# Kernel tuning notes

Measured on AMD Instinct MI355X. Metric: run time of the kernel, lower is better.

## Reference

```python
import jax, jax.numpy as jnp
import numpy as np

K = 3            # pairwise_size
DIL = 2          # pairwise_dilation
COLOR_THR = 0.3  # pairwise_color_thresh
WARMUP = 1.0     # warmup factor (iter >= pairwise_warmup_iters)
COST_CLASS = 1.0
COST_PROJ = 1.0
COST_PAIR = 1.0


def unfold_wo_center(x, k, d):
    # x: (N, T, H, W) -> (N, T, k*k-1, H, W); neighbor at offset (i,j) with dilation d,
    # zero padding, center (i=j=k//2) removed, row-major order (matches F.unfold).
    pad = d * (k - 1) // 2
    H, W = x.shape[-2:]
    xp = jnp.pad(x, ((0, 0), (0, 0), (pad, pad), (pad, pad)))
    outs = []
    for i in range(k):
        for j in range(k):
            if i == k // 2 and j == k // 2:
                continue
            outs.append(xp[..., i * d:i * d + H, j * d:j * d + W])
    return jnp.stack(outs, axis=2)


def batch_dice_loss(inputs, targets):
    # inputs: (N, C), targets: (M, C)
    numerator = 2.0 * jnp.einsum('nc,mc->nm', inputs, targets)
    denominator = inputs.sum(-1)[:, None] + targets.sum(-1)[None, :]
    return 1.0 - (numerator + 1.0) / (denominator + 1.0)


def batch_axis_projection(out_mask, tgt_box_mask, axis):
    # max-project predicted (sigmoid) and box masks along `axis`, dice between projections
    src = jax.nn.sigmoid(out_mask).max(axis=axis).reshape(out_mask.shape[0], -1)
    tgt = tgt_box_mask.max(axis=axis).reshape(tgt_box_mask.shape[0], -1)
    return batch_dice_loss(src, tgt)


def calculate_similarity_cost_video(out_mask, tgt_box_mask, tgt_similarities):
    # out_mask: (Q,T,H,W); tgt_box_mask: (G,T,H,W); tgt_similarities: (G,T,8,H,W)
    Q, T = out_mask.shape[:2]
    G = tgt_box_mask.shape[0]
    tgt_sim = (tgt_similarities >= COLOR_THR).astype(jnp.float32) * tgt_box_mask[:, :, None]
    log_fg = jax.nn.log_sigmoid(out_mask)
    log_bg = jax.nn.log_sigmoid(-out_mask)
    log_fg_u = unfold_wo_center(log_fg, K, DIL)   # (Q,T,8,H,W)
    log_bg_u = unfold_wo_center(log_bg, K, DIL)
    # -log(exp(fg+fg_u) + exp(bg+bg_u)) computed stably
    src_sim = -jnp.logaddexp(log_fg[:, :, None] + log_fg_u,
                             log_bg[:, :, None] + log_bg_u)  # (Q,T,8,H,W)
    src_flat = src_sim.reshape(Q, T, -1)
    tgt_flat = tgt_sim.reshape(G, T, -1)
    numerator = jnp.einsum('qtc,gtc->tqg', src_flat, tgt_flat)      # (T,Q,G)
    denominator = jnp.clip(tgt_flat.sum(-1), 1.0, None)             # (G,T)
    cost = numerator / denominator.T[:, None, :]                    # (T,Q,G)
    return cost.mean(axis=0)                                        # (Q,G)


def setup_inputs() -> dict:
    key = jax.random.key(0)
    k1, k2, k3, k4, k5 = jax.random.split(key, 5)
    Q, G, T, H, W, C = 100, 16, 2, 128, 128, 81
    return {
        'pred_logits': jax.random.normal(k1, (Q, C), dtype=jnp.float32),
        'out_mask': jax.random.normal(k2, (Q, T, H, W), dtype=jnp.float32),
        'tgt_similarities': jax.random.uniform(k3, (G, T, K * K - 1, H, W), dtype=jnp.float32),
        'tgt_ids': jax.random.randint(k4, (G,), 0, C, dtype=jnp.int32),
        'tgt_box_mask': jax.random.randint(k5, (G, T, H, W), 0, 2, dtype=jnp.int32),
    }


def reference(pred_logits, out_mask, tgt_similarities, tgt_ids, tgt_box_mask):
    tgt_box_f = tgt_box_mask.astype(jnp.float32)
    out_prob = jax.nn.softmax(pred_logits, axis=-1)
    cost_class = -out_prob[:, tgt_ids]                                  # (Q,G)
    cost_projection = (batch_axis_projection(out_mask, tgt_box_f, 3)
                       + batch_axis_projection(out_mask, tgt_box_f, 2))  # (Q,G)
    cost_pairwise = calculate_similarity_cost_video(out_mask, tgt_box_f, tgt_similarities) * WARMUP
    C = COST_CLASS * cost_class + COST_PROJ * cost_projection + COST_PAIR * cost_pairwise
    return C
```

## Files before the change

kernel.cpp:

```cpp
#include <hip/hip_runtime.h>
#include <hip/hip_fp16.h>
#include <cstdint>

#define Q_ 100
#define G_ 16
#define T_ 2
#define H_ 128
#define W_ 128
#define HW_ (H_*W_)
#define C_ 81
#define RS_ 69
#define QS_ 553

typedef _Float16 half8 __attribute__((ext_vector_type(8)));
typedef float floatx4 __attribute__((ext_vector_type(4)));

__device__ __forceinline__ float sig_(float x) { return 1.0f / (1.0f + __expf(-x)); }

__launch_bounds__(256)
__global__ void k_prep(const float* __restrict__ om,
                       const int* __restrict__ box,
                       const float* __restrict__ sims,
                       float* __restrict__ srcMW,
                       float* __restrict__ srcMHp,
                       int* __restrict__ tgtMWi,
                       int* __restrict__ tgtMHp,
                       uint32_t* __restrict__ packed,
                       int* __restrict__ cnt_part) {
    __shared__ float credF[128];
    __shared__ int redI[4][4];
    int bid = blockIdx.x;
    int tid = threadIdx.x;

    if (bid < 800) {
        int qt = bid >> 2;
        int rg = bid & 3;
        const float* base = om + (size_t)qt * HW_ + rg * 32 * W_;
        {
            int r = tid >> 3, seg = tid & 7;
            const float4* rp = (const float4*)(base + r * W_ + seg * 16);
            float m = -1e30f;
            #pragma unroll
            for (int i = 0; i < 4; ++i) {
                float4 v = rp[i];
                m = fmaxf(m, fmaxf(fmaxf(v.x, v.y), fmaxf(v.z, v.w)));
            }
            m = fmaxf(m, __shfl_xor(m, 1, 64));
            m = fmaxf(m, __shfl_xor(m, 2, 64));
            m = fmaxf(m, __shfl_xor(m, 4, 64));
            if (seg == 0) srcMW[qt * 128 + rg * 32 + r] = m;
        }
        {
            int c = tid & 127, rh = tid >> 7;
            const float* cp = base + rh * 16 * W_ + c;
            float m = -1e30f;
            #pragma unroll
            for (int i = 0; i < 16; ++i) m = fmaxf(m, cp[i * W_]);
            if (rh == 1) credF[c] = m;
            __syncthreads();
            if (rh == 0) srcMHp[(qt * 4 + rg) * 128 + c] = fmaxf(m, credF[c]);
        }
    } else if (bid < 1056) {
        int b2 = bid - 800;
        int gt = b2 >> 3;
        int rg = b2 & 7;
        const int* base = box + (size_t)gt * HW_ + rg * 16 * W_;
        {
            int r = tid >> 4, seg = tid & 15;
            const int4* rp = (const int4*)(base + r * W_ + seg * 8);
            int4 a = rp[0], b = rp[1];
            int m = max(max(max(a.x, a.y), max(a.z, a.w)),
                        max(max(b.x, b.y), max(b.z, b.w)));
            m = max(m, __shfl_xor(m, 1, 64));
            m = max(m, __shfl_xor(m, 2, 64));
            m = max(m, __shfl_xor(m, 4, 64));
            m = max(m, __shfl_xor(m, 8, 64));
            if (seg == 0) tgtMWi[gt * 128 + rg * 16 + r] = m;
        }
        {
            int* credi = (int*)credF;
            int c = tid & 127, rh = tid >> 7;
            const int* cp = base + rh * 8 * W_ + c;
            int m = 0;
            #pragma unroll
            for (int i = 0; i < 8; ++i) m = max(m, cp[i * W_]);
            if (rh == 1) credi[c] = m;
            __syncthreads();
            if (rh == 0) tgtMHp[(gt * 8 + rg) * 128 + c] = max(m, credi[c]);
        }
    } else {
        int b3 = bid - 1056;
        int gg = b3 & 3;
        int pxblk = b3 >> 2;
        int p0 = pxblk * 512 + tid * 2;
        int t = p0 >> 14;
        int pp = p0 & (HW_ - 1);

        uint32_t w0 = 0, w1 = 0;
        int pc[4];
        #pragma unroll
        for (int b = 0; b < 4; ++b) {
            int g = gg * 4 + b;
            const float* sbase = sims + ((size_t)(g * T_ + t) * 8) * HW_ + pp;
            int2 bx = *(const int2*)(box + (size_t)(g * T_ + t) * HW_ + pp);
            uint32_t by0 = 0, by1 = 0;
            #pragma unroll
            for (int e = 0; e < 8; ++e) {
                float2 sv = *(const float2*)(sbase + (size_t)e * HW_);
                by0 |= (sv.x >= 0.3f ? 1u : 0u) << e;
                by1 |= (sv.y >= 0.3f ? 1u : 0u) << e;
            }
            by0 = bx.x ? by0 : 0u;
            by1 = bx.y ? by1 : 0u;
            w0 |= by0 << (b * 8);
            w1 |= by1 << (b * 8);
            pc[b] = __popc(by0) + __popc(by1);
        }
        *(uint2*)&packed[(size_t)gg * (T_ * HW_) + p0] = make_uint2(w0, w1);

        int wid = tid >> 6, lane = tid & 63;
        #pragma unroll
        for (int b = 0; b < 4; ++b) {
            int s = pc[b];
            #pragma unroll
            for (int o = 32; o > 0; o >>= 1) s += __shfl_down(s, o, 64);
            if (lane == 0) redI[wid][b] = s;
        }
        __syncthreads();
        if (tid < 4)
            cnt_part[pxblk * 16 + gg * 4 + tid] =
                redI[0][tid] + redI[1][tid] + redI[2][tid] + redI[3][tid];
    }
}

__global__ void k_dice(const float* __restrict__ logits, const int* __restrict__ ids,
                       const float* __restrict__ srcMW, const float* __restrict__ srcMHp,
                       const int* __restrict__ tgtMWi, const int* __restrict__ tgtMHp,
                       const int* __restrict__ cnt_part,
                       int* __restrict__ cntF,
                       float* __restrict__ out) {
    int q = blockIdx.x >> 4;
    int g = blockIdx.x & 15;
    int l = threadIdx.x;

    if (q == 0) {
        int tt = l >> 5, pb = l & 31;
        int v = cnt_part[(tt * 32 + pb) * 16 + g];
        #pragma unroll
        for (int o = 1; o <= 16; o <<= 1) v += __shfl_xor(v, o, 64);
        if (pb == 0) cntF[tt * G_ + g] = v;
    }

    float v0 = (l < C_) ? logits[q * C_ + l] : -1e30f;
    float v1 = (l + 64 < C_) ? logits[q * C_ + l + 64] : -1e30f;
    float mx = fmaxf(v0, v1);
    #pragma unroll
    for (int o = 32; o > 0; o >>= 1) mx = fmaxf(mx, __shfl_xor(mx, o, 64));
    float es = ((l < C_) ? __expf(v0 - mx) : 0.0f)
             + ((l + 64 < C_) ? __expf(v1 - mx) : 0.0f);
    #pragma unroll
    for (int o = 32; o > 0; o >>= 1) es += __shfl_xor(es, o, 64);

    float d3 = 0, t3 = 0, s3 = 0, d2 = 0, t2 = 0, s2 = 0;
    #pragma unroll
    for (int i = 0; i < 4; ++i) {
        int c = i * 64 + l;
        int tt = c >> 7, cc = c & 127;
        float sW = sig_(srcMW[(q * 2 + tt) * 128 + cc]);
        float mh = srcMHp[((q * 2 + tt) * 4 + 0) * 128 + cc];
        #pragma unroll
        for (int r = 1; r < 4; ++r)
            mh = fmaxf(mh, srcMHp[((q * 2 + tt) * 4 + r) * 128 + cc]);
        float sH = sig_(mh);
        float tW = (float)tgtMWi[(g * 2 + tt) * 128 + cc];
        int th = tgtMHp[((g * 2 + tt) * 8 + 0) * 128 + cc];
        #pragma unroll
        for (int r = 1; r < 8; ++r)
            th = max(th, tgtMHp[((g * 2 + tt) * 8 + r) * 128 + cc]);
        float tH = (float)th;
        d3 += sW * tW; t3 += tW; s3 += sW;
        d2 += sH * tH; t2 += tH; s2 += sH;
    }
    #pragma unroll
    for (int o = 32; o > 0; o >>= 1) {
        d3 += __shfl_xor(d3, o, 64); t3 += __shfl_xor(t3, o, 64);
        s3 += __shfl_xor(s3, o, 64); d2 += __shfl_xor(d2, o, 64);
        t2 += __shfl_xor(t2, o, 64); s2 += __shfl_xor(s2, o, 64);
    }
    if (l == 0) {
        float p = __expf(logits[q * C_ + ids[g]] - mx) / es;
        float dice3 = 1.0f - (2.0f * d3 + 1.0f) / (s3 + t3 + 1.0f);
        float dice2 = 1.0f - (2.0f * d2 + 1.0f) / (s2 + t2 + 1.0f);
        out[q * G_ + g] = -p + dice3 + dice2;
    }
}

__launch_bounds__(256, 4)
__global__ void k_pair(const float* __restrict__ om,
                       const uint32_t* __restrict__ packed,
                       const int* __restrict__ cntF,
                       float* __restrict__ out) {
    int bid = blockIdx.x;
    int wh = bid & 1;
    int rg = (bid >> 1) & 31;
    int t  = (bid >> 6) & 1;
    int qt = bid >> 7;
    int qbase = qt * 16;
    int rowbase = rg * 4;
    int cbase = wh * 64;
    int tid = threadIdx.x;

    __shared__ uint32_t tile[16 * QS_];

    #pragma unroll
    for (int i = 0; i < 8; ++i) {
        int idx = i * 256 + tid;
        int c4 = idx & 15;
        int row = (idx >> 4) & 7;
        int q = idx >> 7;
        int gq = qbase + q;
        int grow = rowbase - 2 + row;
        float4 x = make_float4(0.f, 0.f, 0.f, 0.f);
        if (gq < Q_ && (unsigned)grow < (unsigned)H_)
            x = *(const float4*)(om + (((size_t)gq * T_ + t) * H_ + grow) * W_ + cbase + c4 * 4);
        uint32_t* dst = &tile[q * QS_ + row * RS_ + 2 + c4 * 4];
        {
            float E = __expf(-x.x); __half2 h = __floats2half2_rn(E, __logf(1.f + E)); dst[0] = *(uint32_t*)&h;
        }{
            float E = __expf(-x.y); __half2 h = __floats2half2_rn(E, __logf(1.f + E)); dst[1] = *(uint32_t*)&h;
        }{
            float E = __expf(-x.z); __half2 h = __floats2half2_rn(E, __logf(1.f + E)); dst[2] = *(uint32_t*)&h;
        }{
            float E = __expf(-x.w); __half2 h = __floats2half2_rn(E, __logf(1.f + E)); dst[3] = *(uint32_t*)&h;
        }
    }
    #pragma unroll
    for (int i = 0; i < 2; ++i) {
        int idx = i * 256 + tid;
        int cc = idx & 3;
        int row = (idx >> 2) & 7;
        int q = idx >> 5;
        int col = (cc < 2) ? cc : cc + 64;
        int gcol = cbase - 2 + col;
        int gq = qbase + q;
        int grow = rowbase - 2 + row;
        float x = 0.f;
        if (gq < Q_ && (unsigned)grow < (unsigned)H_ && (unsigned)gcol < (unsigned)W_)
            x = om[(((size_t)gq * T_ + t) * H_ + grow) * W_ + gcol];
        float E = __expf(-x);
        __half2 h = __floats2half2_rn(E, __logf(1.f + E));
        tile[q * QS_ + row * RS_ + col] = *(uint32_t*)&h;
    }
    __syncthreads();

    int l = tid & 63;
    int w = tid >> 6;
    int mn = l & 15;
    int pq = l >> 4;
    int growS = rowbase + w;

    const uint32_t* pbase = packed + (size_t)(mn >> 2) * (T_ * HW_) + t * HW_
                          + (growS << 7) + cbase + (pq << 4);
    uint4 pkA = *(const uint4*)(pbase + 0);
    uint4 pkB = *(const uint4*)(pbase + 4);
    uint4 pkC = *(const uint4*)(pbase + 8);
    uint4 pkD = *(const uint4*)(pbase + 12);
    uint32_t pkw[16] = {pkA.x, pkA.y, pkA.z, pkA.w, pkB.x, pkB.y, pkB.z, pkB.w,
                        pkC.x, pkC.y, pkC.z, pkC.w, pkD.x, pkD.y, pkD.z, pkD.w};

    const uint32_t* tq = &tile[mn * QS_ + (w + 2) * RS_ + 2 + (pq << 4)];

    bool rowU = (growS >= 2), rowD = (growS <= H_ - 3);
    int bsh = (mn & 3) * 8;

    const int dy[8] = {-2,-2,-2, 0,0, 2,2,2};
    const int dx[8] = {-2, 0, 2,-2,2,-2,0,2};

    floatx4 acc0 = {0.f,0.f,0.f,0.f}, acc1 = {0.f,0.f,0.f,0.f};

    #pragma unroll
    for (int grp = 0; grp < 16; ++grp) {
        int gcol = cbase + (pq << 4) + grp;
        bool colL = (gcol >= 2), colR = (gcol <= W_ - 3);
        bool m8[8] = {rowU && colL, rowU, rowU && colR,
                      colL, colR,
                      rowD && colL, rowD, rowD && colR};

        uint32_t selfw = tq[grp];
        __half2 sh = *(__half2*)&selfw;
        float Ep = __half2float(__low2half(sh));
        float Lp = __half2float(__high2half(sh));
        uint32_t byte = (pkw[grp] >> bsh) & 255u;

        half8 af;
        #pragma unroll
        for (int e = 0; e < 8; ++e) {
            uint32_t nw = tq[grp + dy[e] * RS_ + dx[e]];
            __half2 nh = *(__half2*)&nw;
            float En = __half2float(__low2half(nh));
            float Ln = __half2float(__high2half(nh));
            float s = Lp + Ln - __logf(fmaf(Ep, En, 1.0f));
            s = m8[e] ? s : 0.0f;
            af[e] = (_Float16)s;
        }
        union { half8 h; uint32_t w4[4]; } bfu;
        uint32_t xb = byte | (byte << 15);
        bfu.w4[0] = ((xb >> 0) & 0x10001u) * 0x3C00u;
        bfu.w4[1] = ((xb >> 2) & 0x10001u) * 0x3C00u;
        bfu.w4[2] = ((xb >> 4) & 0x10001u) * 0x3C00u;
        bfu.w4[3] = ((xb >> 6) & 0x10001u) * 0x3C00u;

        if (grp & 1) acc1 = __builtin_amdgcn_mfma_f32_16x16x32_f16(af, bfu.h, acc1, 0, 0, 0);
        else         acc0 = __builtin_amdgcn_mfma_f32_16x16x32_f16(af, bfu.h, acc0, 0, 0, 0);
    }

    __syncthreads();
    float* red = (float*)tile;
    #pragma unroll
    for (int j = 0; j < 4; ++j)
        red[(w * 16 + pq * 4 + j) * 17 + mn] = acc0[j] + acc1[j];
    __syncthreads();
    {
        int row = tid >> 4, g = tid & 15;
        float v = red[(0 * 16 + row) * 17 + g] + red[(1 * 16 + row) * 17 + g]
                + red[(2 * 16 + row) * 17 + g] + red[(3 * 16 + row) * 17 + g];
        int gq = qbase + row;
        if (gq < Q_) {
            int den = max(1, cntF[t * G_ + g]);
            atomicAdd(&out[gq * G_ + g], v * (0.5f / (float)den));
        }
    }
}

extern "C" void kernel_launch(void* const* d_in, const int* in_sizes, int n_in,
                              void* d_out, int out_size, void* d_ws, size_t ws_size,
                              hipStream_t stream) {
    const float* pred_logits = (const float*)d_in[0];
    const float* out_mask    = (const float*)d_in[1];
    const float* sims        = (const float*)d_in[2];
    const int*   tgt_ids     = (const int*)d_in[3];
    const int*   tgt_box     = (const int*)d_in[4];
    float* out = (float*)d_out;

    float*    srcMW    = (float*)d_ws;
    float*    srcMHp   = srcMW + Q_ * T_ * 128;
    int*      tgtMWi   = (int*)(srcMHp + Q_ * T_ * 4 * 128);
    int*      tgtMHp   = tgtMWi + G_ * T_ * 128;
    int*      cnt_part = tgtMHp + G_ * T_ * 8 * 128;
    int*      cntF     = cnt_part + 64 * 16;
    uint32_t* packed   = (uint32_t*)(cntF + G_ * T_);

    k_prep<<<1312, 256, 0, stream>>>(out_mask, tgt_box, sims,
                                     srcMW, srcMHp, tgtMWi, tgtMHp, packed, cnt_part);
    k_dice<<<Q_ * G_, 64, 0, stream>>>(pred_logits, tgt_ids, srcMW, srcMHp,
                                       tgtMWi, tgtMHp, cnt_part, cntF, out);
    k_pair<<<7 * T_ * 32 * 2, 256, 0, stream>>>(out_mask, packed, cntF, out);
}
```

Measured before the change: 113.0 us.

## Merge dice and pairwise kernels into one launch with atomic accumulation

Folds the dice/class-cost kernel into the pairwise kernel as extra blocks, so one fewer launch and no serial dependency between them. The output is zeroed by an extra block in the prep kernel and both paths atomically add into it. Each pairwise block now sums the partial counts itself instead of reading a precomputed cntF. The cost is redundant count reductions per block, plus extra atomics on the output.

```diff
diff --git a/kernel.cpp b/kernel.cpp
--- a/kernel.cpp
+++ b/kernel.cpp
@@ -26,7 +26,8 @@
                        int* __restrict__ tgtMWi,
                        int* __restrict__ tgtMHp,
                        uint32_t* __restrict__ packed,
-                       int* __restrict__ cnt_part) {
+                       int* __restrict__ cnt_part,
+                       float* __restrict__ out) {
     __shared__ float credF[128];
     __shared__ int redI[4][4];
     int bid = blockIdx.x;
@@ -88,7 +89,7 @@
             __syncthreads();
             if (rh == 0) tgtMHp[(gt * 8 + rg) * 128 + c] = max(m, credi[c]);
         }
-    } else {
+    } else if (bid < 1312) {
         int b3 = bid - 1056;
         int gg = b3 & 3;
         int pxblk = b3 >> 2;
@@ -130,204 +131,207 @@
         if (tid < 4)
             cnt_part[pxblk * 16 + gg * 4 + tid] =
                 redI[0][tid] + redI[1][tid] + redI[2][tid] + redI[3][tid];
+    } else {
+        #pragma unroll
+        for (int i = 0; i < 7; ++i) {
+            int idx = i * 256 + tid;
+            if (idx < Q_ * G_) out[idx] = 0.0f;
+        }
     }
 }
 
-__global__ void k_dice(const float* __restrict__ logits, const int* __restrict__ ids,
+__launch_bounds__(256, 4)
+__global__ void k_main(const float* __restrict__ om,
+                       const uint32_t* __restrict__ packed,
+                       const int* __restrict__ cnt_part,
+                       const float* __restrict__ logits, const int* __restrict__ ids,
                        const float* __restrict__ srcMW, const float* __restrict__ srcMHp,
                        const int* __restrict__ tgtMWi, const int* __restrict__ tgtMHp,
-                       const int* __restrict__ cnt_part,
-                       int* __restrict__ cntF,
                        float* __restrict__ out) {
-    int q = blockIdx.x >> 4;
-    int g = blockIdx.x & 15;
-    int l = threadIdx.x;
-
-    if (q == 0) {
-        int tt = l >> 5, pb = l & 31;
-        int v = cnt_part[(tt * 32 + pb) * 16 + g];
-        #pragma unroll
-        for (int o = 1; o <= 16; o <<= 1) v += __shfl_xor(v, o, 64);
-        if (pb == 0) cntF[tt * G_ + g] = v;
-    }
-
-    float v0 = (l < C_) ? logits[q * C_ + l] : -1e30f;
-    float v1 = (l + 64 < C_) ? logits[q * C_ + l + 64] : -1e30f;
-    float mx = fmaxf(v0, v1);
-    #pragma unroll
-    for (int o = 32; o > 0; o >>= 1) mx = fmaxf(mx, __shfl_xor(mx, o, 64));
-    float es = ((l < C_) ? __expf(v0 - mx) : 0.0f)
-             + ((l + 64 < C_) ? __expf(v1 - mx) : 0.0f);
-    #pragma unroll
-    for (int o = 32; o > 0; o >>= 1) es += __shfl_xor(es, o, 64);
-
-    float d3 = 0, t3 = 0, s3 = 0, d2 = 0, t2 = 0, s2 = 0;
-    #pragma unroll
-    for (int i = 0; i < 4; ++i) {
-        int c = i * 64 + l;
-        int tt = c >> 7, cc = c & 127;
-        float sW = sig_(srcMW[(q * 2 + tt) * 128 + cc]);
-        float mh = srcMHp[((q * 2 + tt) * 4 + 0) * 128 + cc];
-        #pragma unroll
-        for (int r = 1; r < 4; ++r)
-            mh = fmaxf(mh, srcMHp[((q * 2 + tt) * 4 + r) * 128 + cc]);
-        float sH = sig_(mh);
-        float tW = (float)tgtMWi[(g * 2 + tt) * 128 + cc];
-        int th = tgtMHp[((g * 2 + tt) * 8 + 0) * 128 + cc];
-        #pragma unroll
-        for (int r = 1; r < 8; ++r)
-            th = max(th, tgtMHp[((g * 2 + tt) * 8 + r) * 128 + cc]);
-        float tH = (float)th;
-        d3 += sW * tW; t3 += tW; s3 += sW;
-        d2 += sH * tH; t2 += tH; s2 += sH;
-    }
-    #pragma unroll
-    for (int o = 32; o > 0; o >>= 1) {
-        d3 += __shfl_xor(d3, o, 64); t3 += __shfl_xor(t3, o, 64);
-        s3 += __shfl_xor(s3, o, 64); d2 += __shfl_xor(d2, o, 64);
-        t2 += __shfl_xor(t2, o, 64); s2 += __shfl_xor(s2, o, 64);
-    }
-    if (l == 0) {
-        float p = __expf(logits[q * C_ + ids[g]] - mx) / es;
-        float dice3 = 1.0f - (2.0f * d3 + 1.0f) / (s3 + t3 + 1.0f);
-        float dice2 = 1.0f - (2.0f * d2 + 1.0f) / (s2 + t2 + 1.0f);
-        out[q * G_ + g] = -p + dice3 + dice2;
-    }
-}
-
-__launch_bounds__(256, 4)
-__global__ void k_pair(const float* __restrict__ om,
-                       const uint32_t* __restrict__ packed,
-                       const int* __restrict__ cntF,
-                       float* __restrict__ out) {
+    __shared__ uint32_t tile[16 * QS_];
+    __shared__ int cntS[16];
     int bid = blockIdx.x;
-    int wh = bid & 1;
-    int rg = (bid >> 1) & 31;
-    int t  = (bid >> 6) & 1;
-    int qt = bid >> 7;
-    int qbase = qt * 16;
-    int rowbase = rg * 4;
-    int cbase = wh * 64;
     int tid = threadIdx.x;
 
-    __shared__ uint32_t tile[16 * QS_];
-
-    #pragma unroll
-    for (int i = 0; i < 8; ++i) {
-        int idx = i * 256 + tid;
-        int c4 = idx & 15;
-        int row = (idx >> 4) & 7;
-        int q = idx >> 7;
-        int gq = qbase + q;
-        int grow = rowbase - 2 + row;
-        float4 x = make_float4(0.f, 0.f, 0.f, 0.f);
-        if (gq < Q_ && (unsigned)grow < (unsigned)H_)
-            x = *(const float4*)(om + (((size_t)gq * T_ + t) * H_ + grow) * W_ + cbase + c4 * 4);
-        uint32_t* dst = &tile[q * QS_ + row * RS_ + 2 + c4 * 4];
-        {
-            float E = __expf(-x.x); __half2 h = __floats2half2_rn(E, __logf(1.f + E)); dst[0] = *(uint32_t*)&h;
-        }{
-            float E = __expf(-x.y); __half2 h = __floats2half2_rn(E, __logf(1.f + E)); dst[1] = *(uint32_t*)&h;
-        }{
-            float E = __expf(-x.z); __half2 h = __floats2half2_rn(E, __logf(1.f + E)); dst[2] = *(uint32_t*)&h;
-        }{
-            float E = __expf(-x.w); __half2 h = __floats2half2_rn(E, __logf(1.f + E)); dst[3] = *(uint32_t*)&h;
-        }
-    }
-    #pragma unroll
-    for (int i = 0; i < 2; ++i) {
-        int idx = i * 256 + tid;
-        int cc = idx & 3;
-        int row = (idx >> 2) & 7;
-        int q = idx >> 5;
-        int col = (cc < 2) ? cc : cc + 64;
-        int gcol = cbase - 2 + col;
-        int gq = qbase + q;
-        int grow = rowbase - 2 + row;
-        float x = 0.f;
-        if (gq < Q_ && (unsigned)grow < (unsigned)H_ && (unsigned)gcol < (unsigned)W_)
-            x = om[(((size_t)gq * T_ + t) * H_ + grow) * W_ + gcol];
-        float E = __expf(-x);
-        __half2 h = __floats2half2_rn(E, __logf(1.f + E));
-        tile[q * QS_ + row * RS_ + col] = *(uint32_t*)&h;
-    }
-    __syncthreads();
-
-    int l = tid & 63;
-    int w = tid >> 6;
-    int mn = l & 15;
-    int pq = l >> 4;
-    int growS = rowbase + w;
-
-    const uint32_t* pbase = packed + (size_t)(mn >> 2) * (T_ * HW_) + t * HW_
-                          + (growS << 7) + cbase + (pq << 4);
-    uint4 pkA = *(const uint4*)(pbase + 0);
-    uint4 pkB = *(const uint4*)(pbase + 4);
-    uint4 pkC = *(const uint4*)(pbase + 8);
-    uint4 pkD = *(const uint4*)(pbase + 12);
-    uint32_t pkw[16] = {pkA.x, pkA.y, pkA.z, pkA.w, pkB.x, pkB.y, pkB.z, pkB.w,
-                        pkC.x, pkC.y, pkC.z, pkC.w, pkD.x, pkD.y, pkD.z, pkD.w};
-
-    const uint32_t* tq = &tile[mn * QS_ + (w + 2) * RS_ + 2 + (pq << 4)];
-
-    bool rowU = (growS >= 2), rowD = (growS <= H_ - 3);
-    int bsh = (mn & 3) * 8;
-
-    const int dy[8] = {-2,-2,-2, 0,0, 2,2,2};
-    const int dx[8] = {-2, 0, 2,-2,2,-2,0,2};
-
-    floatx4 acc0 = {0.f,0.f,0.f,0.f}, acc1 = {0.f,0.f,0.f,0.f};
-
-    #pragma unroll
-    for (int grp = 0; grp < 16; ++grp) {
-        int gcol = cbase + (pq << 4) + grp;
-        bool colL = (gcol >= 2), colR = (gcol <= W_ - 3);
-        bool m8[8] = {rowU && colL, rowU, rowU && colR,
-                      colL, colR,
-                      rowD && colL, rowD, rowD && colR};
-
-        uint32_t selfw = tq[grp];
-        __half2 sh = *(__half2*)&selfw;
-        float Ep = __half2float(__low2half(sh));
-        float Lp = __half2float(__high2half(sh));
-        uint32_t byte = (pkw[grp] >> bsh) & 255u;
-
-        half8 af;
-        #pragma unroll
-        for (int e = 0; e < 8; ++e) {
-            uint32_t nw = tq[grp + dy[e] * RS_ + dx[e]];
-            __half2 nh = *(__half2*)&nw;
-            float En = __half2float(__low2half(nh));
-            float Ln = __half2float(__high2half(nh));
-            float s = Lp + Ln - __logf(fmaf(Ep, En, 1.0f));
-            s = m8[e] ? s : 0.0f;
-            af[e] = (_Float16)s;
-        }
-        union { half8 h; uint32_t w4[4]; } bfu;
-        uint32_t xb = byte | (byte << 15);
-        bfu.w4[0] = ((xb >> 0) & 0x10001u) * 0x3C00u;
-        bfu.w4[1] = ((xb >> 2) & 0x10001u) * 0x3C00u;
-        bfu.w4[2] = ((xb >> 4) & 0x10001u) * 0x3C00u;
-        bfu.w4[3] = ((xb >> 6) & 0x10001u) * 0x3C00u;
-
-        if (grp & 1) acc1 = __builtin_amdgcn_mfma_f32_16x16x32_f16(af, bfu.h, acc1, 0, 0, 0);
-        else         acc0 = __builtin_amdgcn_mfma_f32_16x16x32_f16(af, bfu.h, acc0, 0, 0, 0);
-    }
-
-    __syncthreads();
-    float* red = (float*)tile;
-    #pragma unroll
-    for (int j = 0; j < 4; ++j)
-        red[(w * 16 + pq * 4 + j) * 17 + mn] = acc0[j] + acc1[j];
-    __syncthreads();
-    {
-        int row = tid >> 4, g = tid & 15;
-        float v = red[(0 * 16 + row) * 17 + g] + red[(1 * 16 + row) * 17 + g]
-                + red[(2 * 16 + row) * 17 + g] + red[(3 * 16 + row) * 17 + g];
-        int gq = qbase + row;
-        if (gq < Q_) {
-            int den = max(1, cntF[t * G_ + g]);
-            atomicAdd(&out[gq * G_ + g], v * (0.5f / (float)den));
+    if (bid < 896) {
+        int wh = bid & 1;
+        int rg = (bid >> 1) & 31;
+        int t  = (bid >> 6) & 1;
+        int qt = bid >> 7;
+        int qbase = qt * 16;
+        int rowbase = rg * 4;
+        int cbase = wh * 64;
+
+        #pragma unroll
+        for (int i = 0; i < 8; ++i) {
+            int idx = i * 256 + tid;
+            int c4 = idx & 15;
+            int row = (idx >> 4) & 7;
+            int q = idx >> 7;
+            int gq = qbase + q;
+            int grow = rowbase - 2 + row;
+            float4 x = make_float4(0.f, 0.f, 0.f, 0.f);
+            if (gq < Q_ && (unsigned)grow < (unsigned)H_)
+                x = *(const float4*)(om + (((size_t)gq * T_ + t) * H_ + grow) * W_ + cbase + c4 * 4);
+            uint32_t* dst = &tile[q * QS_ + row * RS_ + 2 + c4 * 4];
+            {
+                float E = __expf(-x.x); __half2 h = __floats2half2_rn(E, __logf(1.f + E)); dst[0] = *(uint32_t*)&h;
+            }{
+                float E = __expf(-x.y); __half2 h = __floats2half2_rn(E, __logf(1.f + E)); dst[1] = *(uint32_t*)&h;
+            }{
+                float E = __expf(-x.z); __half2 h = __floats2half2_rn(E, __logf(1.f + E)); dst[2] = *(uint32_t*)&h;
+            }{
+                float E = __expf(-x.w); __half2 h = __floats2half2_rn(E, __logf(1.f + E)); dst[3] = *(uint32_t*)&h;
+            }
+        }
+        #pragma unroll
+        for (int i = 0; i < 2; ++i) {
+            int idx = i * 256 + tid;
+            int cc = idx & 3;
+            int row = (idx >> 2) & 7;
+            int q = idx >> 5;
+            int col = (cc < 2) ? cc : cc + 64;
+            int gcol = cbase - 2 + col;
+            int gq = qbase + q;
+            int grow = rowbase - 2 + row;
+            float x = 0.f;
+            if (gq < Q_ && (unsigned)grow < (unsigned)H_ && (unsigned)gcol < (unsigned)W_)
+                x = om[(((size_t)gq * T_ + t) * H_ + grow) * W_ + gcol];
+            float E = __expf(-x);
+            __half2 h = __floats2half2_rn(E, __logf(1.f + E));
+            tile[q * QS_ + row * RS_ + col] = *(uint32_t*)&h;
+        }
+        if (tid < 16) {
+            int s = 0;
+            #pragma unroll
+            for (int i = 0; i < 32; ++i) s += cnt_part[(t * 32 + i) * 16 + tid];
+            cntS[tid] = max(1, s);
+        }
+        __syncthreads();
+
+        int l = tid & 63;
+        int w = tid >> 6;
+        int mn = l & 15;
+        int pq = l >> 4;
+        int growS = rowbase + w;
+
+        const uint32_t* pbase = packed + (size_t)(mn >> 2) * (T_ * HW_) + t * HW_
+                              + (growS << 7) + cbase + (pq << 4);
+        uint4 pkA = *(const uint4*)(pbase + 0);
+        uint4 pkB = *(const uint4*)(pbase + 4);
+        uint4 pkC = *(const uint4*)(pbase + 8);
+        uint4 pkD = *(const uint4*)(pbase + 12);
+        uint32_t pkw[16] = {pkA.x, pkA.y, pkA.z, pkA.w, pkB.x, pkB.y, pkB.z, pkB.w,
+                            pkC.x, pkC.y, pkC.z, pkC.w, pkD.x, pkD.y, pkD.z, pkD.w};
+
+        const uint32_t* tq = &tile[mn * QS_ + (w + 2) * RS_ + 2 + (pq << 4)];
+
+        bool rowU = (growS >= 2), rowD = (growS <= H_ - 3);
+        int bsh = (mn & 3) * 8;
+
+        const int dy[8] = {-2,-2,-2, 0,0, 2,2,2};
+        const int dx[8] = {-2, 0, 2,-2,2,-2,0,2};
+
+        floatx4 acc0 = {0.f,0.f,0.f,0.f}, acc1 = {0.f,0.f,0.f,0.f};
+
+        #pragma unroll
+        for (int grp = 0; grp < 16; ++grp) {
+            int gcol = cbase + (pq << 4) + grp;
+            bool colL = (gcol >= 2), colR = (gcol <= W_ - 3);
+            bool m8[8] = {rowU && colL, rowU, rowU && colR,
+                          colL, colR,
+                          rowD && colL, rowD, rowD && colR};
+
+            uint32_t selfw = tq[grp];
+            __half2 sh = *(__half2*)&selfw;
+            float Ep = __half2float(__low2half(sh));
+            float Lp = __half2float(__high2half(sh));
+            uint32_t byte = (pkw[grp] >> bsh) & 255u;
+
+            half8 af;
+            #pragma unroll
+            for (int e = 0; e < 8; ++e) {
+                uint32_t nw = tq[grp + dy[e] * RS_ + dx[e]];
+                __half2 nh = *(__half2*)&nw;
+                float En = __half2float(__low2half(nh));
+                float Ln = __half2float(__high2half(nh));
+                float s = Lp + Ln - __logf(fmaf(Ep, En, 1.0f));
+                s = m8[e] ? s : 0.0f;
+                af[e] = (_Float16)s;
+            }
+            union { half8 h; uint32_t w4[4]; } bfu;
+            uint32_t xb = byte | (byte << 15);
+            bfu.w4[0] = ((xb >> 0) & 0x10001u) * 0x3C00u;
+            bfu.w4[1] = ((xb >> 2) & 0x10001u) * 0x3C00u;
+            bfu.w4[2] = ((xb >> 4) & 0x10001u) * 0x3C00u;
+            bfu.w4[3] = ((xb >> 6) & 0x10001u) * 0x3C00u;
+
+            if (grp & 1) acc1 = __builtin_amdgcn_mfma_f32_16x16x32_f16(af, bfu.h, acc1, 0, 0, 0);
+            else         acc0 = __builtin_amdgcn_mfma_f32_16x16x32_f16(af, bfu.h, acc0, 0, 0, 0);
+        }
+
+        __syncthreads();
+        float* red = (float*)tile;
+        #pragma unroll
+        for (int j = 0; j < 4; ++j)
+            red[(w * 16 + pq * 4 + j) * 17 + mn] = acc0[j] + acc1[j];
+        __syncthreads();
+        {
+            int row = tid >> 4, g = tid & 15;
+            float v = red[(0 * 16 + row) * 17 + g] + red[(1 * 16 + row) * 17 + g]
+                    + red[(2 * 16 + row) * 17 + g] + red[(3 * 16 + row) * 17 + g];
+            int gq = qbase + row;
+            if (gq < Q_)
+                atomicAdd(&out[gq * G_ + g], v * (0.5f / (float)cntS[g]));
+        }
+    } else {
+        int w = tid >> 6;
+        int l = tid & 63;
+        int pr = (bid - 896) * 4 + w;
+        int q = pr >> 4;
+        int g = pr & 15;
+
+        float v0 = (l < C_) ? logits[q * C_ + l] : -1e30f;
+        float v1 = (l + 64 < C_) ? logits[q * C_ + l + 64] : -1e30f;
+        float mx = fmaxf(v0, v1);
+        #pragma unroll
+        for (int o = 32; o > 0; o >>= 1) mx = fmaxf(mx, __shfl_xor(mx, o, 64));
+        float es = ((l < C_) ? __expf(v0 - mx) : 0.0f)
+                 + ((l + 64 < C_) ? __expf(v1 - mx) : 0.0f);
+        #pragma unroll
+        for (int o = 32; o > 0; o >>= 1) es += __shfl_xor(es, o, 64);
+
+        float d3 = 0, t3 = 0, s3 = 0, d2 = 0, t2 = 0, s2 = 0;
+        #pragma unroll
+        for (int i = 0; i < 4; ++i) {
+            int c = i * 64 + l;
+            int tt = c >> 7, cc = c & 127;
+            float sW = sig_(srcMW[(q * 2 + tt) * 128 + cc]);
+            float mh = srcMHp[((q * 2 + tt) * 4 + 0) * 128 + cc];
+            #pragma unroll
+            for (int r = 1; r < 4; ++r)
+                mh = fmaxf(mh, srcMHp[((q * 2 + tt) * 4 + r) * 128 + cc]);
+            float sH = sig_(mh);
+            float tW = (float)tgtMWi[(g * 2 + tt) * 128 + cc];
+            int th = tgtMHp[((g * 2 + tt) * 8 + 0) * 128 + cc];
+            #pragma unroll
+            for (int r = 1; r < 8; ++r)
+                th = max(th, tgtMHp[((g * 2 + tt) * 8 + r) * 128 + cc]);
+            float tH = (float)th;
+            d3 += sW * tW; t3 += tW; s3 += sW;
+            d2 += sH * tH; t2 += tH; s2 += sH;
+        }
+        #pragma unroll
+        for (int o = 32; o > 0; o >>= 1) {
+            d3 += __shfl_xor(d3, o, 64); t3 += __shfl_xor(t3, o, 64);
+            s3 += __shfl_xor(s3, o, 64); d2 += __shfl_xor(d2, o, 64);
+            t2 += __shfl_xor(t2, o, 64); s2 += __shfl_xor(s2, o, 64);
+        }
+        if (l == 0) {
+            float p = __expf(logits[q * C_ + ids[g]] - mx) / es;
+            float dice3 = 1.0f - (2.0f * d3 + 1.0f) / (s3 + t3 + 1.0f);
+            float dice2 = 1.0f - (2.0f * d2 + 1.0f) / (s2 + t2 + 1.0f);
+            atomicAdd(&out[q * G_ + g], -p + dice3 + dice2);
         }
     }
 }
@@ -347,12 +351,10 @@
     int*      tgtMWi   = (int*)(srcMHp + Q_ * T_ * 4 * 128);
     int*      tgtMHp   = tgtMWi + G_ * T_ * 128;
     int*      cnt_part = tgtMHp + G_ * T_ * 8 * 128;
-    int*      cntF     = cnt_part + 64 * 16;
-    uint32_t* packed   = (uint32_t*)(cntF + G_ * T_);
-
-    k_prep<<<1312, 256, 0, stream>>>(out_mask, tgt_box, sims,
-                                     srcMW, srcMHp, tgtMWi, tgtMHp, packed, cnt_part);
-    k_dice<<<Q_ * G_, 64, 0, stream>>>(pred_logits, tgt_ids, srcMW, srcMHp,
-                                       tgtMWi, tgtMHp, cnt_part, cntF, out);
-    k_pair<<<7 * T_ * 32 * 2, 256, 0, stream>>>(out_mask, packed, cntF, out);
+    uint32_t* packed   = (uint32_t*)(cnt_part + 64 * 16);
+
+    k_prep<<<1313, 256, 0, stream>>>(out_mask, tgt_box, sims,
+                                     srcMW, srcMHp, tgtMWi, tgtMHp, packed, cnt_part, out);
+    k_main<<<1296, 256, 0, stream>>>(out_mask, packed, cnt_part, pred_logits, tgt_ids,
+                                     srcMW, srcMHp, tgtMWi, tgtMHp, out);
 }
```

Measured after the change: 110.2 us. -2.5%, faster.
